# Kernel tuning notes

Measured on AMD Instinct MI355X. Metric: run time of the kernel, lower is better.

The kernel has to match this reference:

```python
import jax, jax.numpy as jnp
import numpy as np

DT = 1e-3  # integration step (coeffs[3])
B, T = 512, 8192


def setup_inputs() -> dict:
    key = jax.random.key(0)
    k1, k2, k3, k4 = jax.random.split(key, 4)
    xicovs = jax.random.normal(k1, (B, T, 2, 2), dtype=jnp.float32) * 0.1
    dy = jax.random.normal(k2, (B, T, 2), dtype=jnp.float32) * 0.1
    # learned 2x2 kernel (initializer='uniform' in keras -> small uniform)
    coeffs_A = jax.random.uniform(k3, (2, 2), minval=-0.05, maxval=0.05, dtype=jnp.float32)
    # fixed measurement matrix C (coeffs[0])
    C = jnp.array([[0.5, 0.1], [-0.1, 0.5]], dtype=jnp.float32)
    del k4
    return {"xicovs": xicovs, "dy": dy, "coeffs_A": coeffs_A, "C": C}


def reference(xicovs, dy, coeffs_A, C):
    # xicovs: [B,T,2,2], dy: [B,T,2], coeffs_A/C: [2,2]
    b = xicovs.shape[0]
    x0 = jnp.tile(jnp.array([[1.0, 0.0]], dtype=xicovs.dtype), (b, 1))  # initial_state
    xic_tm = jnp.transpose(xicovs, (1, 0, 2, 3))  # [T,B,2,2] time-major
    dy_tm = jnp.transpose(dy, (1, 0, 2))          # [T,B,2]

    def step(x, inp):
        xic, dyt = inp
        # A - xicov @ C, per batch element
        A_mx = coeffs_A - jnp.einsum('bij,jk->bik', xic, C)
        out = jnp.einsum('ij,bj->bi', C, x) * DT          # emitted output uses prev state
        dx = jnp.einsum('bij,bj->bi', A_mx, x) * DT + jnp.einsum('bij,bj->bi', xic, dyt)
        return x + dx, out

    _, outs = jax.lax.scan(step, x0, (xic_tm, dy_tm))  # outs: [T,B,2]
    return jnp.transpose(outs, (1, 0, 2))  # [B,T,2] (return_sequences=True)
```

## Files before the change

### kernel.cpp

```cpp
#include <hip/hip_runtime.h>

namespace {

constexpr float kDT = 1e-3f;
constexpr int kB = 512;
constexpr int kT = 8192;
constexpr int kThreads = 1024;
constexpr int kWaves = kThreads / 64;
constexpr int kPassSteps = 2 * kThreads;
constexpr int kPasses = kT / kPassSteps;

struct Xf { float a, b, c, d, p, q; };

__device__ __forceinline__ Xf comp(const Xf& e, const Xf& l) {
  Xf o;
  o.a = l.a * e.a + l.b * e.c;
  o.b = l.a * e.b + l.b * e.d;
  o.c = l.c * e.a + l.d * e.c;
  o.d = l.c * e.b + l.d * e.d;
  o.p = l.a * e.p + l.b * e.q + l.p;
  o.q = l.c * e.p + l.d * e.q + l.q;
  return o;
}

__device__ __forceinline__ Xf shfl_up_xf(const Xf& v, int d) {
  Xf r;
  r.a = __shfl_up(v.a, d);
  r.b = __shfl_up(v.b, d);
  r.c = __shfl_up(v.c, d);
  r.d = __shfl_up(v.d, d);
  r.p = __shfl_up(v.p, d);
  r.q = __shfl_up(v.q, d);
  return r;
}

__device__ __forceinline__ Xf make_xf(const float4 xv, float d0, float d1,
                                      float A00, float A01, float A10, float A11,
                                      float C00, float C01, float C10, float C11) {
  Xf m;
  m.a = 1.0f + kDT * (A00 - (xv.x * C00 + xv.y * C10));
  m.b =        kDT * (A01 - (xv.x * C01 + xv.y * C11));
  m.c =        kDT * (A10 - (xv.z * C00 + xv.w * C10));
  m.d = 1.0f + kDT * (A11 - (xv.z * C01 + xv.w * C11));
  m.p = xv.x * d0 + xv.y * d1;
  m.q = xv.z * d0 + xv.w * d1;
  return m;
}

__global__ __launch_bounds__(kThreads) void k_fused(
    const float* __restrict__ xic, const float* __restrict__ dy,
    const float* __restrict__ Ap, const float* __restrict__ Cp,
    float* __restrict__ out) {
  __shared__ float sWT[kWaves][6];
  __shared__ float sWI[kWaves][6];

  const int tid = threadIdx.x;
  const int lane = tid & 63;
  const int w = tid >> 6;
  const size_t rbase = (size_t)blockIdx.x * kT;
  const size_t rbase2 = (size_t)blockIdx.x * (kT / 2);

  const float4* X4 = reinterpret_cast<const float4*>(xic);
  const float4* D4 = reinterpret_cast<const float4*>(dy);
  float4* O4 = reinterpret_cast<float4*>(out);

  const float A00 = Ap[0], A01 = Ap[1], A10 = Ap[2], A11 = Ap[3];
  const float C00 = Cp[0], C01 = Cp[1], C10 = Cp[2], C11 = Cp[3];

  float4 xva[2], xvb[2], dva[2];

  {
    const size_t s = (size_t)2 * tid;
    xva[0] = X4[rbase + s];
    xvb[0] = X4[rbase + s + 1];
    dva[0] = D4[rbase2 + tid];
  }

  float x0 = 1.0f, x1 = 0.0f;

#pragma unroll
  for (int c = 0; c < kPasses; ++c) {
    const int buf = c & 1;
    if (c + 1 < kPasses) {
      const size_t s = (size_t)(c + 1) * kPassSteps + 2 * tid;
      xva[buf ^ 1] = X4[rbase + s];
      xvb[buf ^ 1] = X4[rbase + s + 1];
      dva[buf ^ 1] = D4[rbase2 + (size_t)(c + 1) * kThreads + tid];
    }

    const Xf s0 = make_xf(xva[buf], dva[buf].x, dva[buf].y,
                          A00, A01, A10, A11, C00, C01, C10, C11);
    const Xf s1 = make_xf(xvb[buf], dva[buf].z, dva[buf].w,
                          A00, A01, A10, A11, C00, C01, C10, C11);
    const Xf tot = comp(s0, s1);

    Xf inc = tot;
#pragma unroll
    for (int d = 1; d < 64; d <<= 1) {
      const Xf r = shfl_up_xf(inc, d);
      if (lane >= d) inc = comp(r, inc);
    }

    if (lane == 63) {
      sWT[w][0] = inc.a; sWT[w][1] = inc.b; sWT[w][2] = inc.c;
      sWT[w][3] = inc.d; sWT[w][4] = inc.p; sWT[w][5] = inc.q;
    }
    __syncthreads();

    if (w == 0) {
      Xf v{1.f, 0.f, 0.f, 1.f, 0.f, 0.f};
      if (lane < kWaves) {
        v = Xf{sWT[lane][0], sWT[lane][1], sWT[lane][2],
               sWT[lane][3], sWT[lane][4], sWT[lane][5]};
      }
#pragma unroll
      for (int d = 1; d < kWaves; d <<= 1) {
        const Xf r = shfl_up_xf(v, d);
        if (lane >= d && lane < kWaves) v = comp(r, v);
      }
      if (lane < kWaves) {
        sWI[lane][0] = v.a; sWI[lane][1] = v.b; sWI[lane][2] = v.c;
        sWI[lane][3] = v.d; sWI[lane][4] = v.p; sWI[lane][5] = v.q;
      }
    }
    __syncthreads();

    Xf Ew{1.f, 0.f, 0.f, 1.f, 0.f, 0.f};
    if (w > 0) {
      Ew = Xf{sWI[w - 1][0], sWI[w - 1][1], sWI[w - 1][2],
              sWI[w - 1][3], sWI[w - 1][4], sWI[w - 1][5]};
    }
    Xf le = shfl_up_xf(inc, 1);
    if (lane == 0) le = Xf{1.f, 0.f, 0.f, 1.f, 0.f, 0.f};

    const Xf ex = comp(Ew, le);

    float e0 = ex.a * x0 + ex.b * x1 + ex.p;
    float e1 = ex.c * x0 + ex.d * x1 + ex.q;

    float4 o;
    o.x = kDT * (C00 * e0 + C01 * e1);
    o.y = kDT * (C10 * e0 + C11 * e1);
    const float t0 = s0.a * e0 + s0.b * e1 + s0.p;
    const float t1 = s0.c * e0 + s0.d * e1 + s0.q;
    o.z = kDT * (C00 * t0 + C01 * t1);
    o.w = kDT * (C10 * t0 + C11 * t1);
    O4[rbase2 + (size_t)c * kThreads + tid] = o;

    const Xf T{sWI[kWaves - 1][0], sWI[kWaves - 1][1], sWI[kWaves - 1][2],
               sWI[kWaves - 1][3], sWI[kWaves - 1][4], sWI[kWaves - 1][5]};
    const float n0 = T.a * x0 + T.b * x1 + T.p;
    const float n1 = T.c * x0 + T.d * x1 + T.q;
    x0 = n0; x1 = n1;
  }
}

}

extern "C" void kernel_launch(void* const* d_in, const int* in_sizes, int n_in,
                              void* d_out, int out_size, void* d_ws,
                              size_t ws_size, hipStream_t stream) {
  const float* xic = (const float*)d_in[0];
  const float* dy  = (const float*)d_in[1];
  const float* Ap  = (const float*)d_in[2];
  const float* Cp  = (const float*)d_in[3];
  float* out = (float*)d_out;

  k_fused<<<kB, kThreads, 0, stream>>>(xic, dy, Ap, Cp, out);
}
```

Baseline: 33.85 us.

## Split scan into two-kernel reduce-then-scan across chunked blocks

Replaces the single per-row block that walks four sequential passes with two kernels. The first computes each 512-step chunk's composed affine transform and writes it to workspace. The second recomputes the local scan, folds the preceding chunk totals serially to get the starting state, and emits outputs. This exposes far more blocks (16 per row) to fill the GPU and removes the serial pass loop. The cost is reading the inputs twice, a second launch, and a per-block serial prefix over up to 15 chunk totals.

```diff
diff --git a/kernel.cpp b/kernel.cpp
--- a/kernel.cpp
+++ b/kernel.cpp
@@ -5,10 +5,12 @@
 constexpr float kDT = 1e-3f;
 constexpr int kB = 512;
 constexpr int kT = 8192;
-constexpr int kThreads = 1024;
-constexpr int kWaves = kThreads / 64;
-constexpr int kPassSteps = 2 * kThreads;
-constexpr int kPasses = kT / kPassSteps;
+constexpr int kThr = 256;
+constexpr int kSteps = 2;
+constexpr int kChunk = kThr * kSteps;
+constexpr int kNC = kT / kChunk;
+constexpr int kWaves = kThr / 64;
+constexpr int kBlocks = kB * kNC;
 
 struct Xf { float a, b, c, d, p, q; };
 
@@ -25,12 +27,17 @@
 
 __device__ __forceinline__ Xf shfl_up_xf(const Xf& v, int d) {
   Xf r;
-  r.a = __shfl_up(v.a, d);
-  r.b = __shfl_up(v.b, d);
-  r.c = __shfl_up(v.c, d);
-  r.d = __shfl_up(v.d, d);
-  r.p = __shfl_up(v.p, d);
-  r.q = __shfl_up(v.q, d);
+  r.a = __shfl_up(v.a, d); r.b = __shfl_up(v.b, d);
+  r.c = __shfl_up(v.c, d); r.d = __shfl_up(v.d, d);
+  r.p = __shfl_up(v.p, d); r.q = __shfl_up(v.q, d);
+  return r;
+}
+
+__device__ __forceinline__ Xf shfl_down_xf(const Xf& v, int d) {
+  Xf r;
+  r.a = __shfl_down(v.a, d); r.b = __shfl_down(v.b, d);
+  r.c = __shfl_down(v.c, d); r.d = __shfl_down(v.d, d);
+  r.p = __shfl_down(v.p, d); r.q = __shfl_down(v.q, d);
   return r;
 }
 
@@ -47,18 +54,67 @@
   return m;
 }
 
-__global__ __launch_bounds__(kThreads) void k_fused(
+__global__ __launch_bounds__(kThr) void k_tot(
     const float* __restrict__ xic, const float* __restrict__ dy,
     const float* __restrict__ Ap, const float* __restrict__ Cp,
-    float* __restrict__ out) {
+    float* __restrict__ tot) {
   __shared__ float sWT[kWaves][6];
-  __shared__ float sWI[kWaves][6];
-
   const int tid = threadIdx.x;
   const int lane = tid & 63;
   const int w = tid >> 6;
-  const size_t rbase = (size_t)blockIdx.x * kT;
-  const size_t rbase2 = (size_t)blockIdx.x * (kT / 2);
+  const int blk = blockIdx.x;
+  const size_t step0 = (size_t)blk * kChunk + 2 * tid;
+
+  const float4* X4 = reinterpret_cast<const float4*>(xic);
+  const float4* D4 = reinterpret_cast<const float4*>(dy);
+
+  const float A00 = Ap[0], A01 = Ap[1], A10 = Ap[2], A11 = Ap[3];
+  const float C00 = Cp[0], C01 = Cp[1], C10 = Cp[2], C11 = Cp[3];
+
+  const float4 xv0 = X4[step0];
+  const float4 xv1 = X4[step0 + 1];
+  const float4 dv = D4[step0 >> 1];
+
+  const Xf s0 = make_xf(xv0, dv.x, dv.y, A00, A01, A10, A11, C00, C01, C10, C11);
+  const Xf s1 = make_xf(xv1, dv.z, dv.w, A00, A01, A10, A11, C00, C01, C10, C11);
+  Xf t = comp(s0, s1);
+
+#pragma unroll
+  for (int d = 1; d < 64; d <<= 1) {
+    const Xf r = shfl_down_xf(t, d);
+    t = comp(t, r);
+  }
+  if (lane == 0) {
+    sWT[w][0] = t.a; sWT[w][1] = t.b; sWT[w][2] = t.c;
+    sWT[w][3] = t.d; sWT[w][4] = t.p; sWT[w][5] = t.q;
+  }
+  __syncthreads();
+
+  if (tid == 0) {
+    Xf pre{sWT[0][0], sWT[0][1], sWT[0][2], sWT[0][3], sWT[0][4], sWT[0][5]};
+    for (int i = 1; i < kWaves; ++i) {
+      const Xf wt{sWT[i][0], sWT[i][1], sWT[i][2],
+                  sWT[i][3], sWT[i][4], sWT[i][5]};
+      pre = comp(pre, wt);
+    }
+    float* o = tot + (size_t)blk * 6;
+    o[0] = pre.a; o[1] = pre.b; o[2] = pre.c;
+    o[3] = pre.d; o[4] = pre.p; o[5] = pre.q;
+  }
+}
+
+__global__ __launch_bounds__(kThr) void k_emit(
+    const float* __restrict__ xic, const float* __restrict__ dy,
+    const float* __restrict__ Ap, const float* __restrict__ Cp,
+    const float* __restrict__ tot, float* __restrict__ out) {
+  __shared__ float sWT[kWaves][6];
+  const int tid = threadIdx.x;
+  const int lane = tid & 63;
+  const int w = tid >> 6;
+  const int blk = blockIdx.x;
+  const int r = blk / kNC;
+  const int c = blk % kNC;
+  const size_t step0 = (size_t)blk * kChunk + 2 * tid;
 
   const float4* X4 = reinterpret_cast<const float4*>(xic);
   const float4* D4 = reinterpret_cast<const float4*>(dy);
@@ -67,92 +123,60 @@
   const float A00 = Ap[0], A01 = Ap[1], A10 = Ap[2], A11 = Ap[3];
   const float C00 = Cp[0], C01 = Cp[1], C10 = Cp[2], C11 = Cp[3];
 
-  float4 xva[2], xvb[2], dva[2];
+  const float4 xv0 = X4[step0];
+  const float4 xv1 = X4[step0 + 1];
+  const float4 dv = D4[step0 >> 1];
 
+  float e0 = 1.0f, e1 = 0.0f;
   {
-    const size_t s = (size_t)2 * tid;
-    xva[0] = X4[rbase + s];
-    xvb[0] = X4[rbase + s + 1];
-    dva[0] = D4[rbase2 + tid];
+    Xf pre{1.f, 0.f, 0.f, 1.f, 0.f, 0.f};
+    const float* tr = tot + (size_t)r * kNC * 6;
+    for (int i = 0; i < c; ++i) {
+      const Xf ti{tr[i * 6 + 0], tr[i * 6 + 1], tr[i * 6 + 2],
+                  tr[i * 6 + 3], tr[i * 6 + 4], tr[i * 6 + 5]};
+      pre = comp(pre, ti);
+    }
+    e0 = pre.a + pre.p;
+    e1 = pre.c + pre.q;
   }
 
-  float x0 = 1.0f, x1 = 0.0f;
+  const Xf s0 = make_xf(xv0, dv.x, dv.y, A00, A01, A10, A11, C00, C01, C10, C11);
+  const Xf s1 = make_xf(xv1, dv.z, dv.w, A00, A01, A10, A11, C00, C01, C10, C11);
+  const Xf tt = comp(s0, s1);
 
+  Xf inc = tt;
 #pragma unroll
-  for (int c = 0; c < kPasses; ++c) {
-    const int buf = c & 1;
-    if (c + 1 < kPasses) {
-      const size_t s = (size_t)(c + 1) * kPassSteps + 2 * tid;
-      xva[buf ^ 1] = X4[rbase + s];
-      xvb[buf ^ 1] = X4[rbase + s + 1];
-      dva[buf ^ 1] = D4[rbase2 + (size_t)(c + 1) * kThreads + tid];
-    }
+  for (int d = 1; d < 64; d <<= 1) {
+    const Xf rr = shfl_up_xf(inc, d);
+    if (lane >= d) inc = comp(rr, inc);
+  }
+  if (lane == 63) {
+    sWT[w][0] = inc.a; sWT[w][1] = inc.b; sWT[w][2] = inc.c;
+    sWT[w][3] = inc.d; sWT[w][4] = inc.p; sWT[w][5] = inc.q;
+  }
+  __syncthreads();
 
-    const Xf s0 = make_xf(xva[buf], dva[buf].x, dva[buf].y,
-                          A00, A01, A10, A11, C00, C01, C10, C11);
-    const Xf s1 = make_xf(xvb[buf], dva[buf].z, dva[buf].w,
-                          A00, A01, A10, A11, C00, C01, C10, C11);
-    const Xf tot = comp(s0, s1);
+  Xf Ew{1.f, 0.f, 0.f, 1.f, 0.f, 0.f};
+  for (int i = 0; i < w; ++i) {
+    const Xf wt{sWT[i][0], sWT[i][1], sWT[i][2],
+                sWT[i][3], sWT[i][4], sWT[i][5]};
+    Ew = comp(Ew, wt);
+  }
+  Xf le = shfl_up_xf(inc, 1);
+  if (lane == 0) le = Xf{1.f, 0.f, 0.f, 1.f, 0.f, 0.f};
+  const Xf ex = comp(Ew, le);
 
-    Xf inc = tot;
-#pragma unroll
-    for (int d = 1; d < 64; d <<= 1) {
-      const Xf r = shfl_up_xf(inc, d);
-      if (lane >= d) inc = comp(r, inc);
-    }
+  const float x0 = ex.a * e0 + ex.b * e1 + ex.p;
+  const float x1 = ex.c * e0 + ex.d * e1 + ex.q;
 
-    if (lane == 63) {
-      sWT[w][0] = inc.a; sWT[w][1] = inc.b; sWT[w][2] = inc.c;
-      sWT[w][3] = inc.d; sWT[w][4] = inc.p; sWT[w][5] = inc.q;
-    }
-    __syncthreads();
-
-    if (w == 0) {
-      Xf v{1.f, 0.f, 0.f, 1.f, 0.f, 0.f};
-      if (lane < kWaves) {
-        v = Xf{sWT[lane][0], sWT[lane][1], sWT[lane][2],
-               sWT[lane][3], sWT[lane][4], sWT[lane][5]};
-      }
-#pragma unroll
-      for (int d = 1; d < kWaves; d <<= 1) {
-        const Xf r = shfl_up_xf(v, d);
-        if (lane >= d && lane < kWaves) v = comp(r, v);
-      }
-      if (lane < kWaves) {
-        sWI[lane][0] = v.a; sWI[lane][1] = v.b; sWI[lane][2] = v.c;
-        sWI[lane][3] = v.d; sWI[lane][4] = v.p; sWI[lane][5] = v.q;
-      }
-    }
-    __syncthreads();
-
-    Xf Ew{1.f, 0.f, 0.f, 1.f, 0.f, 0.f};
-    if (w > 0) {
-      Ew = Xf{sWI[w - 1][0], sWI[w - 1][1], sWI[w - 1][2],
-              sWI[w - 1][3], sWI[w - 1][4], sWI[w - 1][5]};
-    }
-    Xf le = shfl_up_xf(inc, 1);
-    if (lane == 0) le = Xf{1.f, 0.f, 0.f, 1.f, 0.f, 0.f};
-
-    const Xf ex = comp(Ew, le);
-
-    float e0 = ex.a * x0 + ex.b * x1 + ex.p;
-    float e1 = ex.c * x0 + ex.d * x1 + ex.q;
-
-    float4 o;
-    o.x = kDT * (C00 * e0 + C01 * e1);
-    o.y = kDT * (C10 * e0 + C11 * e1);
-    const float t0 = s0.a * e0 + s0.b * e1 + s0.p;
-    const float t1 = s0.c * e0 + s0.d * e1 + s0.q;
-    o.z = kDT * (C00 * t0 + C01 * t1);
-    o.w = kDT * (C10 * t0 + C11 * t1);
-    O4[rbase2 + (size_t)c * kThreads + tid] = o;
-
-    const Xf T{sWI[kWaves - 1][0], sWI[kWaves - 1][1], sWI[kWaves - 1][2],
-               sWI[kWaves - 1][3], sWI[kWaves - 1][4], sWI[kWaves - 1][5]};
-    const float n0 = T.a * x0 + T.b * x1 + T.p;
-    const float n1 = T.c * x0 + T.d * x1 + T.q;
-    x0 = n0; x1 = n1;
-  }
+  float4 o;
+  o.x = kDT * (C00 * x0 + C01 * x1);
+  o.y = kDT * (C10 * x0 + C11 * x1);
+  const float t0 = s0.a * x0 + s0.b * x1 + s0.p;
+  const float t1 = s0.c * x0 + s0.d * x1 + s0.q;
+  o.z = kDT * (C00 * t0 + C01 * t1);
+  o.w = kDT * (C10 * t0 + C11 * t1);
+  O4[step0 >> 1] = o;
 }
 
 }
@@ -166,5 +190,8 @@
   const float* Cp  = (const float*)d_in[3];
   float* out = (float*)d_out;
 
-  k_fused<<<kB, kThreads, 0, stream>>>(xic, dy, Ap, Cp, out);
+  float* tot = (float*)d_ws;
+
+  k_tot<<<kBlocks, kThr, 0, stream>>>(xic, dy, Ap, Cp, tot);
+  k_emit<<<kBlocks, kThr, 0, stream>>>(xic, dy, Ap, Cp, tot, out);
 }
```

Result: slower. 49.91 us (+47.4%).
